# Performance work log

Measured on AMD Instinct MI355X. Metric: run time of the kernel, lower is better.

Reference implementation:

```python
import jax, jax.numpy as jnp
import numpy as np


def _gcn_conv(x, W, b, row, col, norm, num_nodes):
    # PyG GCNConv: transform then normalized sum-aggregate over edges (incl. self loops)
    xw = x @ W                                   # [N, F_out]
    msg = xw[row] * norm[:, None]                # gather + scale, [E+N, F_out]
    agg = jax.ops.segment_sum(msg, col, num_segments=num_nodes)
    return agg + b


def setup_inputs() -> dict:
    key = jax.random.key(0)
    ks = jax.random.split(key, 10)
    N, E, F_in, H = 100000, 1600000, 128, 128
    Hh = H // 2
    x = jax.random.normal(ks[0], (N, F_in), dtype=jnp.float32)
    edge_index = jax.random.randint(ks[1], (2, E), 0, N, dtype=jnp.int64)
    def glorot(k, shape):
        lim = float(np.sqrt(6.0 / (shape[0] + shape[1])))
        return jax.random.uniform(k, shape, dtype=jnp.float32, minval=-lim, maxval=lim)
    return {
        "x": x,
        "edge_index": edge_index,
        "W1": glorot(ks[2], (F_in, Hh)), "b1": jnp.zeros((Hh,), jnp.float32),
        "Wf1": glorot(ks[3], (F_in, Hh)), "bf1": jnp.zeros((Hh,), jnp.float32),
        "W2": glorot(ks[4], (H, 1)), "b2": jnp.zeros((1,), jnp.float32),
        "Wf2": glorot(ks[5], (H, 1)), "bf2": jnp.zeros((1,), jnp.float32),
    }


def reference(x, edge_index, W1, b1, Wf1, bf1, W2, b2, Wf2, bf2):
    N = x.shape[0]
    loop = jnp.arange(N, dtype=edge_index.dtype)
    row = jnp.concatenate([edge_index[0], loop])   # sources
    col = jnp.concatenate([edge_index[1], loop])   # targets
    # symmetric normalization D^{-1/2} (A+I) D^{-1/2}, degree on target nodes
    deg = jax.ops.segment_sum(jnp.ones_like(col, dtype=x.dtype), col, num_segments=N)
    dinv = jnp.where(deg > 0, jax.lax.rsqrt(deg), 0.0)
    norm = dinv[row] * dinv[col]                   # [E+N]
    h = jnp.concatenate([
        _gcn_conv(x, W1, b1, row, col, norm, N),
        x @ Wf1 + bf1,
    ], axis=1)
    h = jax.nn.relu(h)
    # dropout is identity in eval mode
    out = _gcn_conv(h, W2, b2, row, col, norm, N) + (h @ Wf2 + bf2)
    return out.reshape(-1)
```

## Files before the change

kernel.cpp:

```cpp
#include <hip/hip_runtime.h>
#include <hip/hip_fp16.h>

constexpr int FIN   = 128;
constexpr int HH    = 64;
constexpr int NPB   = 256;
constexpr int MAXNB = 512;
constexpr int BCH   = 4096;
constexpr int BCAP  = 4608;
constexpr int CAPB  = 4500;

typedef _Float16 half4v __attribute__((ext_vector_type(4)));
typedef _Float16 half8v __attribute__((ext_vector_type(8)));
typedef float    f32x4 __attribute__((ext_vector_type(4)));

__global__ __launch_bounds__(256) void k_gemm(
    const float* __restrict__ x, const float* __restrict__ W1,
    const float* __restrict__ Wf1, _Float16* __restrict__ xwh, int N)
{
    __shared__ _Float16 wt[128 * 128];

    const int tid = threadIdx.x;
    for (int idx = tid; idx < 128 * 128; idx += 256) {
        int n = idx & 127, k = idx >> 7;
        float v = (n < HH) ? W1[k * HH + n] : Wf1[k * HH + (n - HH)];
        int g  = k >> 3, j = k & 7;
        int pg = g ^ (n & 7);
        wt[n * 128 + pg * 8 + j] = (_Float16)v;
    }
    __syncthreads();

    const int w  = tid >> 6;
    const int l  = tid & 63;
    const int rb = blockIdx.x * 64 + w * 16;

    int arow = rb + (l & 15);
    arow = (arow < N) ? arow : (N - 1);
    half8v af[4];
#pragma unroll
    for (int ks = 0; ks < 4; ++ks) {
        const float* src = x + (size_t)arow * FIN + ks * 32 + (l >> 4) * 8;
        float4 x0 = *(const float4*)(src);
        float4 x1 = *(const float4*)(src + 4);
        half8v a;
        a[0] = (_Float16)x0.x; a[1] = (_Float16)x0.y;
        a[2] = (_Float16)x0.z; a[3] = (_Float16)x0.w;
        a[4] = (_Float16)x1.x; a[5] = (_Float16)x1.y;
        a[6] = (_Float16)x1.z; a[7] = (_Float16)x1.w;
        af[ks] = a;
    }

    const int orow0 = rb + (l >> 4) * 4;
#pragma unroll
    for (int c = 0; c < 8; ++c) {
        f32x4 acc = {0.f, 0.f, 0.f, 0.f};
        const int n = (l & 15) + c * 16;
#pragma unroll
        for (int ks = 0; ks < 4; ++ks) {
            int g  = ks * 4 + (l >> 4);
            int pg = g ^ (n & 7);
            half8v bf = *(const half8v*)(wt + n * 128 + pg * 8);
            acc = __builtin_amdgcn_mfma_f32_16x16x32_f16(af[ks], bf, acc, 0, 0, 0);
        }
        const int ocol = c * 16 + (l & 15);
#pragma unroll
        for (int r = 0; r < 4; ++r) {
            int orow = orow0 + r;
            if (orow < N)
                xwh[(size_t)orow * FIN + ocol] = (_Float16)acc[r];
        }
    }
}

__global__ __launch_bounds__(256) void k_bin(
    const int* __restrict__ ei, int* __restrict__ bcur,
    int* __restrict__ binned, int E, int NB)
{
    __shared__ int hist[MAXNB], scur[MAXNB], gbase[MAXNB], sbase[MAXNB];
    __shared__ int ssum[256];
    __shared__ int2 st[BCH];
    const int tid = threadIdx.x;
    const int e0  = blockIdx.x * BCH;
    const int nE  = min(BCH, E - e0);

    for (int b = tid; b < NB; b += 256) hist[b] = 0;
    __syncthreads();

    for (int k = tid; k < nE; k += 256)
        atomicAdd(&hist[ei[E + e0 + k] >> 8], 1);
    __syncthreads();

    int h0 = (2 * tid     < NB) ? hist[2 * tid]     : 0;
    int h1 = (2 * tid + 1 < NB) ? hist[2 * tid + 1] : 0;
    ssum[tid] = h0 + h1;
    __syncthreads();
    for (int o = 1; o < 256; o <<= 1) {
        int y = (tid >= o) ? ssum[tid - o] : 0;
        __syncthreads();
        ssum[tid] += y;
        __syncthreads();
    }
    int eb = ssum[tid] - h0 - h1;
    if (2 * tid     < NB) { sbase[2 * tid]     = eb;      scur[2 * tid]     = eb; }
    if (2 * tid + 1 < NB) { sbase[2 * tid + 1] = eb + h0; scur[2 * tid + 1] = eb + h0; }
    __syncthreads();

    for (int b = tid; b < NB; b += 256)
        if (hist[b] > 0) gbase[b] = atomicAdd(bcur + b, hist[b]);

    for (int k = tid; k < nE; k += 256) {
        int r = ei[e0 + k];
        int c = ei[E + e0 + k];
        int s = atomicAdd(&scur[c >> 8], 1);
        st[s] = make_int2(r, c);
    }
    __syncthreads();

    for (int s = tid; s < nE; s += 256) {
        int2 rc = st[s];
        int b = rc.y >> 8;
        long dest = (long)b * BCAP + gbase[b] + (s - sbase[b]);
        binned[dest] = ((rc.y & 255) << 24) | rc.x;
    }
}

__global__ __launch_bounds__(256) void k_bscan(
    const int* __restrict__ bcur, int* __restrict__ bbase, int NB)
{
    __shared__ int s[256];
    const int t = threadIdx.x;
    int a = (2 * t     < NB) ? bcur[2 * t]     : 0;
    int b = (2 * t + 1 < NB) ? bcur[2 * t + 1] : 0;
    s[t] = a + b;
    __syncthreads();
    for (int o = 1; o < 256; o <<= 1) {
        int y = (t >= o) ? s[t - o] : 0;
        __syncthreads();
        s[t] += y;
        __syncthreads();
    }
    int excl = s[t] - a - b;
    if (2 * t     < NB) bbase[2 * t]     = excl;
    if (2 * t + 1 < NB) bbase[2 * t + 1] = excl + a;
}

__global__ __launch_bounds__(256) void k_place(
    const int* __restrict__ binned, const int* __restrict__ bcur,
    const int* __restrict__ bbase, int* __restrict__ cnt, int* __restrict__ off,
    float* __restrict__ dinv, int* __restrict__ sedge, int N)
{
    const int b   = blockIdx.x;
    const int tid = threadIdx.x;
    const int nlo = b << 8;
    const int nn  = min(NPB, N - nlo);
    __shared__ int lcnt[NPB], loff[NPB], lscan[NPB];
    __shared__ int stage[CAPB];
    lcnt[tid] = 0;
    __syncthreads();
    const int ke = bcur[b];
    const int* src = binned + (long)b * BCAP;
    for (int k = tid; k < ke; k += 256)
        atomicAdd(&lcnt[((unsigned)src[k]) >> 24], 1);
    __syncthreads();
    int v = lcnt[tid];
    lscan[tid] = v;
    __syncthreads();
    for (int o = 1; o < 256; o <<= 1) {
        int y = (tid >= o) ? lscan[tid - o] : 0;
        __syncthreads();
        lscan[tid] += y;
        __syncthreads();
    }
    int excl = lscan[tid] - v;
    loff[tid] = excl;
    const int base = bbase[b];
    if (tid < nn) {
        cnt[nlo + tid]  = v;
        off[nlo + tid]  = base + excl;
        dinv[nlo + tid] = rsqrtf((float)v + 1.0f);
    }
    lcnt[tid] = 0;
    __syncthreads();
    if (ke <= CAPB) {
        for (int k = tid; k < ke; k += 256) {
            int p  = src[k];
            int li = ((unsigned)p) >> 24;
            int q  = atomicAdd(&lcnt[li], 1);
            stage[loff[li] + q] = p & 0x00FFFFFF;
        }
        __syncthreads();
        for (int s = tid; s < ke; s += 256) sedge[base + s] = stage[s];
    } else {
        for (int k = tid; k < ke; k += 256) {
            int p  = src[k];
            int li = ((unsigned)p) >> 24;
            int q  = atomicAdd(&lcnt[li], 1);
            sedge[base + loff[li] + q] = p & 0x00FFFFFF;
        }
    }
}

__global__ __launch_bounds__(256) void k_fused(
    const int* __restrict__ off, const int* __restrict__ cnt,
    const int* __restrict__ sedge, const float* __restrict__ dinv,
    const _Float16* __restrict__ xwh,
    const float* __restrict__ b1, const float* __restrict__ bf1,
    const float* __restrict__ W2, const float* __restrict__ Wf2,
    const float* __restrict__ b2, const float* __restrict__ bf2,
    float* __restrict__ z, float* __restrict__ out, int N)
{
    const int wv   = (blockIdx.x * blockDim.x + threadIdx.x) >> 6;
    const int lane = threadIdx.x & 63;
    const int g    = lane >> 4;
    const int l16  = lane & 15;
    int i = wv * 4 + g;
    const bool ok = (i < N);
    i = ok ? i : (N - 1);

    const int jb  = off[i];
    const int deg = cnt[i];
    const float di = dinv[i];

    float4 acc = make_float4(0.f, 0.f, 0.f, 0.f);
    int j = 0;
    for (; j + 4 <= deg; j += 4) {
        int r0 = sedge[jb + j];
        int r1 = sedge[jb + j + 1];
        int r2 = sedge[jb + j + 2];
        int r3 = sedge[jb + j + 3];
        float s0 = dinv[r0] * di;
        float s1 = dinv[r1] * di;
        float s2 = dinv[r2] * di;
        float s3 = dinv[r3] * di;
        half4v a0 = *(const half4v*)(xwh + (size_t)r0 * FIN + l16 * 4);
        half4v a1 = *(const half4v*)(xwh + (size_t)r1 * FIN + l16 * 4);
        half4v a2 = *(const half4v*)(xwh + (size_t)r2 * FIN + l16 * 4);
        half4v a3 = *(const half4v*)(xwh + (size_t)r3 * FIN + l16 * 4);
        acc.x = fmaf((float)a0[0], s0, acc.x);
        acc.y = fmaf((float)a0[1], s0, acc.y);
        acc.z = fmaf((float)a0[2], s0, acc.z);
        acc.w = fmaf((float)a0[3], s0, acc.w);
        acc.x = fmaf((float)a1[0], s1, acc.x);
        acc.y = fmaf((float)a1[1], s1, acc.y);
        acc.z = fmaf((float)a1[2], s1, acc.z);
        acc.w = fmaf((float)a1[3], s1, acc.w);
        acc.x = fmaf((float)a2[0], s2, acc.x);
        acc.y = fmaf((float)a2[1], s2, acc.y);
        acc.z = fmaf((float)a2[2], s2, acc.z);
        acc.w = fmaf((float)a2[3], s2, acc.w);
        acc.x = fmaf((float)a3[0], s3, acc.x);
        acc.y = fmaf((float)a3[1], s3, acc.y);
        acc.z = fmaf((float)a3[2], s3, acc.z);
        acc.w = fmaf((float)a3[3], s3, acc.w);
    }
    for (; j < deg; ++j) {
        int r = sedge[jb + j];
        float s = dinv[r] * di;
        half4v a = *(const half4v*)(xwh + (size_t)r * FIN + l16 * 4);
        acc.x = fmaf((float)a[0], s, acc.x);
        acc.y = fmaf((float)a[1], s, acc.y);
        acc.z = fmaf((float)a[2], s, acc.z);
        acc.w = fmaf((float)a[3], s, acc.w);
    }

    float dd = di * di;
    half4v svh = *(const half4v*)(xwh + (size_t)i * FIN + l16 * 4);
    acc.x = fmaf((float)svh[0], dd, acc.x);
    acc.y = fmaf((float)svh[1], dd, acc.y);
    acc.z = fmaf((float)svh[2], dd, acc.z);
    acc.w = fmaf((float)svh[3], dd, acc.w);

    float4 b1v  = *(const float4*)(b1  + l16 * 4);
    float4 bf1v = *(const float4*)(bf1 + l16 * 4);
    half4v x1h  = *(const half4v*)(xwh + (size_t)i * FIN + HH + l16 * 4);
    float4 h0, h1;
    h0.x = fmaxf(acc.x + b1v.x, 0.f);  h0.y = fmaxf(acc.y + b1v.y, 0.f);
    h0.z = fmaxf(acc.z + b1v.z, 0.f);  h0.w = fmaxf(acc.w + b1v.w, 0.f);
    h1.x = fmaxf((float)x1h[0] + bf1v.x, 0.f);  h1.y = fmaxf((float)x1h[1] + bf1v.y, 0.f);
    h1.z = fmaxf((float)x1h[2] + bf1v.z, 0.f);  h1.w = fmaxf((float)x1h[3] + bf1v.w, 0.f);

    float4 w2a  = *(const float4*)(W2  + l16 * 4);
    float4 w2b  = *(const float4*)(W2  + HH + l16 * 4);
    float4 wf2a = *(const float4*)(Wf2 + l16 * 4);
    float4 wf2b = *(const float4*)(Wf2 + HH + l16 * 4);

    float zp = h0.x * w2a.x + h0.y * w2a.y + h0.z * w2a.z + h0.w * w2a.w
             + h1.x * w2b.x + h1.y * w2b.y + h1.z * w2b.z + h1.w * w2b.w;
    float fp = h0.x * wf2a.x + h0.y * wf2a.y + h0.z * wf2a.z + h0.w * wf2a.w
             + h1.x * wf2b.x + h1.y * wf2b.y + h1.z * wf2b.z + h1.w * wf2b.w;
#pragma unroll
    for (int o = 8; o > 0; o >>= 1) {
        zp += __shfl_xor(zp, o, 16);
        fp += __shfl_xor(fp, o, 16);
    }
    if (l16 == 0 && ok) {
        z[i]   = zp;
        out[i] = fp + b2[0] + bf2[0];
    }
}

__global__ __launch_bounds__(256) void k_agg2(
    const int* __restrict__ off, const int* __restrict__ cnt,
    const int* __restrict__ sedge, const float* __restrict__ dinv,
    const float* __restrict__ z, float* __restrict__ out, int N)
{
    const int wid  = (blockIdx.x * blockDim.x + threadIdx.x) >> 6;
    const int lane = threadIdx.x & 63;
    const int g    = lane >> 4;
    const int l16  = lane & 15;
    int i = wid * 4 + g;
    bool ok = (i < N);
    i = ok ? i : (N - 1);

    const int jb = off[i], je = jb + cnt[i];
    float s = 0.0f;
    for (int j = jb + l16; j < je; j += 16) {
        int r = sedge[j];
        s = fmaf(z[r], dinv[r], s);
    }
#pragma unroll
    for (int o = 8; o > 0; o >>= 1) s += __shfl_xor(s, o, 64);
    if (l16 == 0 && ok) {
        float di = dinv[i];
        out[i] += di * fmaf(z[i], di, s);
    }
}

extern "C" void kernel_launch(void* const* d_in, const int* in_sizes, int n_in,
                              void* d_out, int out_size, void* d_ws, size_t ws_size,
                              hipStream_t stream)
{
    const float* x   = (const float*)d_in[0];
    const int*   ei  = (const int*)d_in[1];
    const float* W1  = (const float*)d_in[2];
    const float* b1  = (const float*)d_in[3];
    const float* Wf1 = (const float*)d_in[4];
    const float* bf1 = (const float*)d_in[5];
    const float* W2  = (const float*)d_in[6];
    const float* b2  = (const float*)d_in[7];
    const float* Wf2 = (const float*)d_in[8];
    const float* bf2 = (const float*)d_in[9];

    const int N = in_sizes[0] / FIN;
    const int E = in_sizes[1] / 2;
    const int NB = (N + NPB - 1) / NPB;
    float* out = (float*)d_out;

    float* ws   = (float*)d_ws;
    float* dinv = ws;
    float* z    = dinv + N;
    int*   cnt  = (int*)(z + N);
    int*   bcur = cnt + N;
    int*   bbase = bcur + MAXNB;
    int*   off  = bbase + MAXNB;
    int*   sedge = off + N;
    _Float16* xwh = (_Float16*)(sedge + E);
    int*   binned = (int*)(xwh + (size_t)N * FIN);

    hipMemsetAsync(bcur, 0, (size_t)MAXNB * sizeof(int), stream);

    k_bin<<<(E + BCH - 1) / BCH, 256, 0, stream>>>(ei, bcur, binned, E, NB);
    k_bscan<<<1, 256, 0, stream>>>(bcur, bbase, NB);
    k_place<<<NB, 256, 0, stream>>>(binned, bcur, bbase, cnt, off, dinv, sedge, N);

    k_gemm<<<(N + 63) / 64, 256, 0, stream>>>(x, W1, Wf1, xwh, N);

    {
        long waves = ((long)N + 3) / 4;
        int blocks = (int)((waves * 64 + 255) / 256);
        k_fused<<<blocks, 256, 0, stream>>>(off, cnt, sedge, dinv, xwh,
                                            b1, bf1, W2, Wf2, b2, bf2, z, out, N);
    }

    {
        long waves = ((long)N + 3) / 4;
        int blocks = (int)((waves * 64 + 255) / 256);
        k_agg2<<<blocks, 256, 0, stream>>>(off, cnt, sedge, dinv, z, out, N);
    }
}
```

Measured before the change: 212.8 us.

## Merge edge binning and feature GEMM into one launch to overlap them

Combines the edge-binning kernel and the x@W GEMM kernel into a single launch. Block IDs below nbin do binning and the rest do the GEMM, with the two sharing one union shared-memory buffer. The two stages are independent, so the GPU can run memory-bound binning blocks alongside MFMA GEMM blocks and drop one launch and one stage boundary. The cost is that both roles get the larger shared-memory footprint and the register budget of whichever path needs more, which may reduce occupancy.

```diff
diff --git a/kernel.cpp b/kernel.cpp
--- a/kernel.cpp
+++ b/kernel.cpp
@@ -9,117 +9,123 @@
 constexpr int BCAP  = 4608;
 constexpr int CAPB  = 4500;
 
+constexpr int SMEM_BYTES = BCH * 8 + 4 * MAXNB * 4 + 256 * 4;
+
 typedef _Float16 half4v __attribute__((ext_vector_type(4)));
 typedef _Float16 half8v __attribute__((ext_vector_type(8)));
 typedef float    f32x4 __attribute__((ext_vector_type(4)));
 
-__global__ __launch_bounds__(256) void k_gemm(
+__global__ __launch_bounds__(256) void k_bingemm(
+    const int* __restrict__ ei, int* __restrict__ bcur,
+    int* __restrict__ binned, int E, int NB, int nbin,
     const float* __restrict__ x, const float* __restrict__ W1,
     const float* __restrict__ Wf1, _Float16* __restrict__ xwh, int N)
 {
-    __shared__ _Float16 wt[128 * 128];
-
+    __shared__ __align__(16) char smem[SMEM_BYTES];
     const int tid = threadIdx.x;
-    for (int idx = tid; idx < 128 * 128; idx += 256) {
-        int n = idx & 127, k = idx >> 7;
-        float v = (n < HH) ? W1[k * HH + n] : Wf1[k * HH + (n - HH)];
-        int g  = k >> 3, j = k & 7;
-        int pg = g ^ (n & 7);
-        wt[n * 128 + pg * 8 + j] = (_Float16)v;
-    }
-    __syncthreads();
-
-    const int w  = tid >> 6;
-    const int l  = tid & 63;
-    const int rb = blockIdx.x * 64 + w * 16;
-
-    int arow = rb + (l & 15);
-    arow = (arow < N) ? arow : (N - 1);
-    half8v af[4];
-#pragma unroll
-    for (int ks = 0; ks < 4; ++ks) {
-        const float* src = x + (size_t)arow * FIN + ks * 32 + (l >> 4) * 8;
-        float4 x0 = *(const float4*)(src);
-        float4 x1 = *(const float4*)(src + 4);
-        half8v a;
-        a[0] = (_Float16)x0.x; a[1] = (_Float16)x0.y;
-        a[2] = (_Float16)x0.z; a[3] = (_Float16)x0.w;
-        a[4] = (_Float16)x1.x; a[5] = (_Float16)x1.y;
-        a[6] = (_Float16)x1.z; a[7] = (_Float16)x1.w;
-        af[ks] = a;
-    }
-
-    const int orow0 = rb + (l >> 4) * 4;
-#pragma unroll
-    for (int c = 0; c < 8; ++c) {
-        f32x4 acc = {0.f, 0.f, 0.f, 0.f};
-        const int n = (l & 15) + c * 16;
+
+    if (blockIdx.x < nbin) {
+        int2* st   = (int2*)smem;
+        int* hist  = (int*)(smem + BCH * 8);
+        int* scur  = hist + MAXNB;
+        int* gbase = scur + MAXNB;
+        int* sbase = gbase + MAXNB;
+        int* ssum  = sbase + MAXNB;
+
+        const int e0 = blockIdx.x * BCH;
+        const int nE = min(BCH, E - e0);
+
+        for (int b = tid; b < NB; b += 256) hist[b] = 0;
+        __syncthreads();
+
+        for (int k = tid; k < nE; k += 256)
+            atomicAdd(&hist[ei[E + e0 + k] >> 8], 1);
+        __syncthreads();
+
+        int h0 = (2 * tid     < NB) ? hist[2 * tid]     : 0;
+        int h1 = (2 * tid + 1 < NB) ? hist[2 * tid + 1] : 0;
+        ssum[tid] = h0 + h1;
+        __syncthreads();
+        for (int o = 1; o < 256; o <<= 1) {
+            int y = (tid >= o) ? ssum[tid - o] : 0;
+            __syncthreads();
+            ssum[tid] += y;
+            __syncthreads();
+        }
+        int eb = ssum[tid] - h0 - h1;
+        if (2 * tid     < NB) { sbase[2 * tid]     = eb;      scur[2 * tid]     = eb; }
+        if (2 * tid + 1 < NB) { sbase[2 * tid + 1] = eb + h0; scur[2 * tid + 1] = eb + h0; }
+        __syncthreads();
+
+        for (int b = tid; b < NB; b += 256)
+            if (hist[b] > 0) gbase[b] = atomicAdd(bcur + b, hist[b]);
+
+        for (int k = tid; k < nE; k += 256) {
+            int r = ei[e0 + k];
+            int c = ei[E + e0 + k];
+            int s = atomicAdd(&scur[c >> 8], 1);
+            st[s] = make_int2(r, c);
+        }
+        __syncthreads();
+
+        for (int s = tid; s < nE; s += 256) {
+            int2 rc = st[s];
+            int b = rc.y >> 8;
+            long dest = (long)b * BCAP + gbase[b] + (s - sbase[b]);
+            binned[dest] = ((rc.y & 255) << 24) | rc.x;
+        }
+    } else {
+        _Float16* wt = (_Float16*)smem;
+
+        for (int idx = tid; idx < 128 * 128; idx += 256) {
+            int n = idx & 127, k = idx >> 7;
+            float v = (n < HH) ? W1[k * HH + n] : Wf1[k * HH + (n - HH)];
+            int g  = k >> 3, j = k & 7;
+            int pg = g ^ (n & 7);
+            wt[n * 128 + pg * 8 + j] = (_Float16)v;
+        }
+        __syncthreads();
+
+        const int w  = tid >> 6;
+        const int l  = tid & 63;
+        const int rb = (blockIdx.x - nbin) * 64 + w * 16;
+
+        int arow = rb + (l & 15);
+        arow = (arow < N) ? arow : (N - 1);
+        half8v af[4];
 #pragma unroll
         for (int ks = 0; ks < 4; ++ks) {
-            int g  = ks * 4 + (l >> 4);
-            int pg = g ^ (n & 7);
-            half8v bf = *(const half8v*)(wt + n * 128 + pg * 8);
-            acc = __builtin_amdgcn_mfma_f32_16x16x32_f16(af[ks], bf, acc, 0, 0, 0);
-        }
-        const int ocol = c * 16 + (l & 15);
-#pragma unroll
-        for (int r = 0; r < 4; ++r) {
-            int orow = orow0 + r;
-            if (orow < N)
-                xwh[(size_t)orow * FIN + ocol] = (_Float16)acc[r];
-        }
-    }
-}
-
-__global__ __launch_bounds__(256) void k_bin(
-    const int* __restrict__ ei, int* __restrict__ bcur,
-    int* __restrict__ binned, int E, int NB)
-{
-    __shared__ int hist[MAXNB], scur[MAXNB], gbase[MAXNB], sbase[MAXNB];
-    __shared__ int ssum[256];
-    __shared__ int2 st[BCH];
-    const int tid = threadIdx.x;
-    const int e0  = blockIdx.x * BCH;
-    const int nE  = min(BCH, E - e0);
-
-    for (int b = tid; b < NB; b += 256) hist[b] = 0;
-    __syncthreads();
-
-    for (int k = tid; k < nE; k += 256)
-        atomicAdd(&hist[ei[E + e0 + k] >> 8], 1);
-    __syncthreads();
-
-    int h0 = (2 * tid     < NB) ? hist[2 * tid]     : 0;
-    int h1 = (2 * tid + 1 < NB) ? hist[2 * tid + 1] : 0;
-    ssum[tid] = h0 + h1;
-    __syncthreads();
-    for (int o = 1; o < 256; o <<= 1) {
-        int y = (tid >= o) ? ssum[tid - o] : 0;
-        __syncthreads();
-        ssum[tid] += y;
-        __syncthreads();
-    }
-    int eb = ssum[tid] - h0 - h1;
-    if (2 * tid     < NB) { sbase[2 * tid]     = eb;      scur[2 * tid]     = eb; }
-    if (2 * tid + 1 < NB) { sbase[2 * tid + 1] = eb + h0; scur[2 * tid + 1] = eb + h0; }
-    __syncthreads();
-
-    for (int b = tid; b < NB; b += 256)
-        if (hist[b] > 0) gbase[b] = atomicAdd(bcur + b, hist[b]);
-
-    for (int k = tid; k < nE; k += 256) {
-        int r = ei[e0 + k];
-        int c = ei[E + e0 + k];
-        int s = atomicAdd(&scur[c >> 8], 1);
-        st[s] = make_int2(r, c);
-    }
-    __syncthreads();
-
-    for (int s = tid; s < nE; s += 256) {
-        int2 rc = st[s];
-        int b = rc.y >> 8;
-        long dest = (long)b * BCAP + gbase[b] + (s - sbase[b]);
-        binned[dest] = ((rc.y & 255) << 24) | rc.x;
+            const float* src = x + (size_t)arow * FIN + ks * 32 + (l >> 4) * 8;
+            float4 x0 = *(const float4*)(src);
+            float4 x1 = *(const float4*)(src + 4);
+            half8v a;
+            a[0] = (_Float16)x0.x; a[1] = (_Float16)x0.y;
+            a[2] = (_Float16)x0.z; a[3] = (_Float16)x0.w;
+            a[4] = (_Float16)x1.x; a[5] = (_Float16)x1.y;
+            a[6] = (_Float16)x1.z; a[7] = (_Float16)x1.w;
+            af[ks] = a;
+        }
+
+        const int orow0 = rb + (l >> 4) * 4;
+#pragma unroll
+        for (int c = 0; c < 8; ++c) {
+            f32x4 acc = {0.f, 0.f, 0.f, 0.f};
+            const int n = (l & 15) + c * 16;
+#pragma unroll
+            for (int ks = 0; ks < 4; ++ks) {
+                int g  = ks * 4 + (l >> 4);
+                int pg = g ^ (n & 7);
+                half8v bf = *(const half8v*)(wt + n * 128 + pg * 8);
+                acc = __builtin_amdgcn_mfma_f32_16x16x32_f16(af[ks], bf, acc, 0, 0, 0);
+            }
+            const int ocol = c * 16 + (l & 15);
+#pragma unroll
+            for (int r = 0; r < 4; ++r) {
+                int orow = orow0 + r;
+                if (orow < N)
+                    xwh[(size_t)orow * FIN + ocol] = (_Float16)acc[r];
+            }
+        }
     }
 }
 
@@ -358,11 +364,15 @@
 
     hipMemsetAsync(bcur, 0, (size_t)MAXNB * sizeof(int), stream);
 
-    k_bin<<<(E + BCH - 1) / BCH, 256, 0, stream>>>(ei, bcur, binned, E, NB);
+    {
+        int nbin  = (E + BCH - 1) / BCH;
+        int ngemm = (N + 63) / 64;
+        k_bingemm<<<nbin + ngemm, 256, 0, stream>>>(
+            ei, bcur, binned, E, NB, nbin, x, W1, Wf1, xwh, N);
+    }
+
     k_bscan<<<1, 256, 0, stream>>>(bcur, bbase, NB);
     k_place<<<NB, 256, 0, stream>>>(binned, bcur, bbase, cnt, off, dinv, sedge, N);
-
-    k_gemm<<<(N + 63) / 64, 256, 0, stream>>>(x, W1, Wf1, xwh, N);
 
     {
         long waves = ((long)N + 3) / 4;
```

New measurement: 206.5 us. -3.0%, faster.
